# Optimization experiments

Hardware: AMD Instinct MI355X
Metric: run time of the kernel (lower is better)

The kernel has to match this reference:

```python
import jax, jax.numpy as jnp
import numpy as np

B, C, H, W = 2, 4, 32, 256   # batch, num_classes (class 0 = background), range-image H x W
N = H * W                    # candidate points per (batch, class)
RADIUS = 3.0
KM_ITERS = 1
COORD_SCALE = 60.0           # spread lidar x/y so radius-3 NMS is non-trivial


def setup_inputs() -> dict:
    key = jax.random.key(0)
    k1, k2 = jax.random.split(key)
    segmented_channels = jax.random.normal(k1, (B, C, H, W), dtype=jnp.float32)
    lidar = jax.random.normal(k2, (B, 2, H, W), dtype=jnp.float32) * COORD_SCALE
    return {"segmented_channels": segmented_channels, "lidar": lidar}


def _radius_nms(points, mask, radius):
    # Greedy radius NMS in index order: keep point i iff no earlier kept point
    # lies within `radius`. Masked-out points are never kept (keep init = mask).
    n = points.shape[0]
    idx = jnp.arange(n)
    r2 = radius * radius

    def step(keep, i):
        d2 = jnp.sum((points - points[i]) ** 2, axis=-1)       # [N]
        suppress = keep & (d2 < r2) & (idx > i) & keep[i]
        return keep & ~suppress, None

    keep, _ = jax.lax.scan(step, mask, idx)
    return keep


def _kmeans(points, mask, keep, iters):
    # Centers initialized at the NMS-kept points (same index space as points).
    # Each valid class point is assigned to nearest valid center; centers move
    # to the mean of their assigned points.
    n = points.shape[0]
    centers = points
    w = mask.astype(points.dtype)
    BIG = jnp.asarray(1e30, points.dtype)
    for _ in range(iters):
        d2 = jnp.sum((points[:, None, :] - centers[None, :, :]) ** 2, axis=-1)  # [N,N]
        d2 = jnp.where(keep[None, :], d2, BIG)
        assign = jnp.argmin(d2, axis=1)                         # [N]
        sums = jax.ops.segment_sum(points * w[:, None], assign, num_segments=n)
        cnt = jax.ops.segment_sum(w, assign, num_segments=n)
        upd = sums / jnp.maximum(cnt, 1.0)[:, None]
        centers = jnp.where((keep & (cnt > 0))[:, None], upd, centers)
    return centers * keep[:, None].astype(points.dtype)


def reference(segmented_channels, lidar):
    ind = jnp.argmax(segmented_channels, axis=1)                # [B,H,W] class id per cell
    pts = jnp.stack([lidar[:, 0], lidar[:, 1]], axis=-1).reshape(B, N, 2)
    # boolean class masks for foreground classes 1..C-1
    cls_mask = jnp.stack([ind == c for c in range(1, C)], axis=1).reshape(B, C - 1, N)
    pts_all = jnp.broadcast_to(pts[:, None], (B, C - 1, N, 2)).reshape(B * (C - 1), N, 2)
    mask_all = cls_mask.reshape(B * (C - 1), N)

    def per_bc(args):
        p, m = args
        keep = _radius_nms(p, m, RADIUS)
        centers = _kmeans(p, m, keep, KM_ITERS)
        return centers, keep

    centers, keep = jax.lax.map(per_bc, (pts_all, mask_all))
    # centers: padded [B, C-1, N, 2]; keep marks which rows are real detections
    return centers.reshape(B, C - 1, N, 2), keep.reshape(B, C - 1, N)
```

## Files before the change

kernel.cpp:

```cpp
#include <hip/hip_runtime.h>

#define NPTS 8192
#define BCLS 4
#define NP   6
#define R2   9.0f
#define RAD  3.0f
#define GRD  64
#define NCELL (GRD*GRD)
#define PCAP 2048
#define LDSK 2048

#define ST_U 0u
#define ST_A 1u
#define ST_D 2u

__global__ __launch_bounds__(1024) void k_fused(
    const float* __restrict__ seg, const float* __restrict__ lidar,
    float* __restrict__ sumx, float* __restrict__ sumy, float* __restrict__ cntw,
    float* __restrict__ out)
{
    const int p = blockIdx.x;
    const int b = p / 3, cls = p % 3 + 1;
    const int tid = threadIdx.x, lane = tid & 63, wv = tid >> 6;
    const int base = p * NPTS;

    __shared__ float2 sps[NPTS];
    __shared__ unsigned int cmb[NPTS];
    __shared__ unsigned int cellpack[NCELL];
    __shared__ unsigned short plist[2][PCAP];
    __shared__ float ksx[LDSK], ksy[LDSK], kcn[LDSK];
    __shared__ int pcnt[2];
    __shared__ unsigned long long ballots[128];
    __shared__ unsigned int base128[128];
    __shared__ unsigned int wtot[16];
    __shared__ float redbuf[4][16];
    __shared__ float sbminx, sbminy, scell;
    __shared__ int sM, sK;

    float* ok = out + (size_t)2 * NP * NPTS + base;

    for (int k = tid; k < NPTS; k += 1024) { cmb[k] = ST_U; ok[k] = 0.f; }
    {
        float2* oc = (float2*)(out + (size_t)2 * base);
        for (int k = tid; k < NPTS; k += 1024) oc[k] = make_float2(0.f, 0.f);
    }
    for (int k = tid; k < NCELL; k += 1024) cellpack[k] = 0u;
    for (int k = tid; k < LDSK; k += 1024) { ksx[k] = 0.f; ksy[k] = 0.f; kcn[k] = 0.f; }
    if (tid == 0) { pcnt[0] = 0; pcnt[1] = 0; }

    const float* segb = seg + (size_t)b * BCLS * NPTS;
    const float* lx = lidar + (size_t)b * 2 * NPTS;
    const float* ly = lx + NPTS;
    for (int c0 = 0; c0 < 8; ++c0) {
        int n = c0 * 1024 + tid;
        float bv = segb[n];
        int bc = 0;
        #pragma unroll
        for (int c2 = 1; c2 < BCLS; ++c2) {
            float v = segb[c2 * NPTS + n];
            if (v > bv) { bv = v; bc = c2; }
        }
        unsigned long long bal = __ballot(bc == cls);
        if (lane == 0) ballots[c0 * 16 + wv] = bal;
    }
    for (int n = tid; n < NPTS; n += 1024) sps[n] = make_float2(lx[n], ly[n]);
    __syncthreads();
    if (wv == 0) {
        unsigned int s = (unsigned int)__popcll(ballots[2 * lane]) +
                         (unsigned int)__popcll(ballots[2 * lane + 1]);
        for (int d = 1; d < 64; d <<= 1) s += __shfl_xor(s, d, 64);
        if (lane == 0) sM = (int)s;
    }

    const unsigned long long mw = ballots[tid >> 3];
    {
        float mnx = 3e38f, mxx = -3e38f, mny = 3e38f, mxy = -3e38f;
        #pragma unroll
        for (int q = 0; q < 8; ++q) {
            int n = tid * 8 + q;
            bool m = (mw >> (((tid & 7) << 3) + q)) & 1ull;
            float2 c = sps[n];
            if (m) {
                mnx = fminf(mnx, c.x); mxx = fmaxf(mxx, c.x);
                mny = fminf(mny, c.y); mxy = fmaxf(mxy, c.y);
            }
        }
        for (int d = 32; d; d >>= 1) {
            mnx = fminf(mnx, __shfl_xor(mnx, d, 64));
            mxx = fmaxf(mxx, __shfl_xor(mxx, d, 64));
            mny = fminf(mny, __shfl_xor(mny, d, 64));
            mxy = fmaxf(mxy, __shfl_xor(mxy, d, 64));
        }
        if (lane == 0) { redbuf[0][wv] = mnx; redbuf[1][wv] = mxx;
                         redbuf[2][wv] = mny; redbuf[3][wv] = mxy; }
    }
    __syncthreads();
    if (tid == 0) {
        float a = redbuf[0][0], b2 = redbuf[1][0], c = redbuf[2][0], d = redbuf[3][0];
        for (int q = 1; q < 16; ++q) {
            a = fminf(a, redbuf[0][q]); b2 = fmaxf(b2, redbuf[1][q]);
            c = fminf(c, redbuf[2][q]); d = fmaxf(d, redbuf[3][q]);
        }
        sbminx = a; sbminy = c;
        scell = fmaxf(2.0f * RAD, fmaxf(b2 - a, d - c) / 63.0f);
    }
    __syncthreads();
    const float bminx = sbminx, bminy = sbminy, inv = 1.0f / scell;
    const int M = sM;

    float xq[8], yq[8];
    int cellq[8];
    #pragma unroll
    for (int q = 0; q < 8; ++q) {
        int n = tid * 8 + q;
        bool m = (mw >> (((tid & 7) << 3) + q)) & 1ull;
        float2 c = sps[n];
        xq[q] = c.x; yq[q] = c.y;
        int ix = min(GRD - 1, max(0, (int)((c.x - bminx) * inv)));
        int iy = min(GRD - 1, max(0, (int)((c.y - bminy) * inv)));
        cellq[q] = m ? (iy * GRD + ix) : -1;
        if (m) atomicAdd(&cellpack[iy * GRD + ix], 1u);
    }
    __syncthreads();
    {
        unsigned int c4[4], t4 = 0;
        #pragma unroll
        for (int q = 0; q < 4; ++q) { c4[q] = cellpack[tid * 4 + q]; t4 += c4[q]; }
        unsigned int v = t4;
        for (int d = 1; d < 64; d <<= 1) {
            unsigned int u = __shfl_up(v, d, 64);
            if (lane >= d) v += u;
        }
        if (lane == 63) wtot[wv] = v;
        __syncthreads();
        if (tid == 0) {
            unsigned int acc = 0;
            for (int q = 0; q < 16; ++q) { unsigned int t = wtot[q]; wtot[q] = acc; acc += t; }
        }
        __syncthreads();
        unsigned int excl = wtot[wv] + v - t4;
        #pragma unroll
        for (int q = 0; q < 4; ++q) { cellpack[tid * 4 + q] = excl << 16; excl += c4[q]; }
    }
    __syncthreads();
    #pragma unroll
    for (int q = 0; q < 8; ++q) {
        if (cellq[q] >= 0) {
            unsigned int old = atomicAdd(&cellpack[cellq[q]], 1u);
            unsigned int pos = (old >> 16) + (old & 0xffffu);
            sps[pos] = make_float2(xq[q], yq[q]);
            cmb[pos] = ((unsigned int)(tid * 8 + q) << 2) | ST_U;
        }
    }
    __syncthreads();

    #define ROW_FLAGS(CY, CX0, CX1, NI, ME, DEAD, UNDEC)                          \
    {                                                                             \
        unsigned int wa = cellpack[(CY) * GRD + (CX0)];                           \
        unsigned int wb = cellpack[(CY) * GRD + (CX1)];                           \
        unsigned int f0 = wa >> 16, f1 = (wb >> 16) + (wb & 0xffffu);             \
        for (unsigned int f = f0; f < f1; ++f) {                                  \
            unsigned int wf = cmb[f];                                             \
            float2 q = sps[f];                                                    \
            float dx = __fsub_rn((ME).x, q.x), dy = __fsub_rn((ME).y, q.y);       \
            float d2 = __fadd_rn(__fmul_rn(dx, dx), __fmul_rn(dy, dy));           \
            bool in = (d2 < R2) & ((int)(wf >> 2) < (NI));                        \
            DEAD  |= in & ((wf & 3u) == ST_A);                                    \
            UNDEC |= in & ((wf & 3u) == ST_U);                                    \
        }                                                                         \
    }
    #define SCAN_FLAGS(NI, ME, DEAD, UNDEC)                                       \
    {                                                                             \
        int cx0 = max(0, (int)(((ME).x - RAD - bminx) * inv));                    \
        int cx1 = min(GRD - 1, (int)(((ME).x + RAD - bminx) * inv));              \
        int cy0 = max(0, (int)(((ME).y - RAD - bminy) * inv));                    \
        int cy1 = min(GRD - 1, (int)(((ME).y + RAD - bminy) * inv));              \
        DEAD = false; UNDEC = false;                                              \
        ROW_FLAGS(cy0, cx0, cx1, NI, ME, DEAD, UNDEC);                            \
        if (cy1 > cy0) ROW_FLAGS(cy1, cx0, cx1, NI, ME, DEAD, UNDEC);             \
    }

    for (int e = tid; e < M; e += 1024) {
        unsigned int w = cmb[e];
        int ni = (int)(w >> 2);
        float2 me = sps[e];
        bool dead, undec;
        SCAN_FLAGS(ni, me, dead, undec);
        if (dead) cmb[e] = (w & ~3u) | ST_D;
        else if (!undec) cmb[e] = (w & ~3u) | ST_A;
        bool pendf = !dead && undec;
        unsigned long long act = __ballot(true);
        unsigned long long bal = __ballot(pendf);
        int leader = __builtin_ctzll(act);
        int cnt = __popcll(bal);
        int wbase = 0;
        if (lane == leader && cnt) wbase = atomicAdd(&pcnt[0], cnt);
        wbase = __shfl(wbase, leader, 64);
        if (pendf) {
            int pos = wbase + __popcll(bal & ((1ull << lane) - 1ull));
            if (pos < PCAP) plist[0][pos] = (unsigned short)e;
        }
    }

    int cur = 0;
    for (int round = 0; round < NPTS; ++round) {
        __syncthreads();
        int pc = pcnt[cur];
        if (pc == 0) break;
        if (pc > PCAP) {
            for (;;) {
                bool any = false;
                __syncthreads();
                for (int e = tid; e < M; e += 1024) {
                    unsigned int w = cmb[e];
                    if ((w & 3u) != ST_U) continue;
                    int ni = (int)(w >> 2);
                    float2 me = sps[e];
                    bool dead, undec;
                    SCAN_FLAGS(ni, me, dead, undec);
                    if (dead) cmb[e] = (w & ~3u) | ST_D;
                    else if (!undec) cmb[e] = (w & ~3u) | ST_A;
                    else any = true;
                }
                if (__syncthreads_count(any) == 0) break;
            }
            break;
        }
        if (tid == 0) pcnt[cur ^ 1] = 0;
        __syncthreads();
        for (int idx = tid; idx < pc; idx += 1024) {
            int e = plist[cur][idx];
            unsigned int w = cmb[e];
            int ni = (int)(w >> 2);
            float2 me = sps[e];
            bool dead, undec;
            SCAN_FLAGS(ni, me, dead, undec);
            if (dead) cmb[e] = (w & ~3u) | ST_D;
            else if (!undec) cmb[e] = (w & ~3u) | ST_A;
            bool pendf = !dead && undec;
            unsigned long long act = __ballot(true);
            unsigned long long bal = __ballot(pendf);
            int leader = __builtin_ctzll(act);
            int cnt = __popcll(bal);
            int wbase = 0;
            if (lane == leader && cnt) wbase = atomicAdd(&pcnt[cur ^ 1], cnt);
            wbase = __shfl(wbase, leader, 64);
            if (pendf) {
                int pos = wbase + __popcll(bal & ((1ull << lane) - 1ull));
                if (pos < PCAP) plist[cur ^ 1][pos] = (unsigned short)e;
            }
        }
        cur ^= 1;
    }
    __syncthreads();

    for (int k = 0; k < 8; ++k) {
        int e = (k << 10) + tid;
        unsigned long long bal = __ballot((cmb[e] & 3u) == ST_A);
        if (lane == 0) ballots[(k << 4) + wv] = bal;
    }
    __syncthreads();
    if (wv == 0) {
        unsigned int p0 = (unsigned int)__popcll(ballots[2 * lane]);
        unsigned int p1 = (unsigned int)__popcll(ballots[2 * lane + 1]);
        unsigned int s = p0 + p1, v = s;
        for (int d = 1; d < 64; d <<= 1) {
            unsigned int u = __shfl_up(v, d, 64);
            if (lane >= d) v += u;
        }
        base128[2 * lane] = v - s;
        base128[2 * lane + 1] = v - p1;
        if (lane == 63) sK = (int)v;
    }
    __syncthreads();
    #define KRANK(E) ((int)base128[(E) >> 6] +                                    \
                      __popcll(ballots[(E) >> 6] & ((1ull << ((E) & 63)) - 1ull)))
    if (sK > LDSK) {
        for (int k = tid; k < NPTS; k += 1024) {
            sumx[base + k] = 0.f; sumy[base + k] = 0.f; cntw[base + k] = 0.f;
        }
        __syncthreads();
    }

    #define ROW_ARGMIN(CY, CX0, CX1, ME, BD, BE, BN)                              \
    {                                                                             \
        unsigned int wa = cellpack[(CY) * GRD + (CX0)];                           \
        unsigned int wb = cellpack[(CY) * GRD + (CX1)];                           \
        unsigned int f0 = wa >> 16, f1 = (wb >> 16) + (wb & 0xffffu);             \
        for (unsigned int f = f0; f < f1; ++f) {                                  \
            unsigned int wf = cmb[f];                                             \
            float2 q = sps[f];                                                    \
            float dx = __fsub_rn((ME).x, q.x), dy = __fsub_rn((ME).y, q.y);       \
            float d2 = __fadd_rn(__fmul_rn(dx, dx), __fmul_rn(dy, dy));           \
            int nf = (int)(wf >> 2);                                              \
            bool better = ((wf & 3u) == ST_A) &                                   \
                          ((d2 < BD) | ((d2 == BD) & (nf < BN)));                 \
            BD = better ? d2 : BD;                                                \
            BE = better ? (int)f : BE;                                            \
            BN = better ? nf : BN;                                                \
        }                                                                         \
    }
    for (int e = tid; e < M; e += 1024) {
        unsigned int w = cmb[e];
        float2 me = sps[e];
        int be;
        if ((w & 3u) == ST_A) {
            be = e;
        } else {
            int cx0 = max(0, (int)((me.x - RAD - bminx) * inv));
            int cx1 = min(GRD - 1, (int)((me.x + RAD - bminx) * inv));
            int cy0 = max(0, (int)((me.y - RAD - bminy) * inv));
            int cy1 = min(GRD - 1, (int)((me.y + RAD - bminy) * inv));
            float bd = 3e38f;
            be = -1;
            int bn = 1 << 30;
            ROW_ARGMIN(cy0, cx0, cx1, me, bd, be, bn);
            if (cy1 > cy0) ROW_ARGMIN(cy1, cx0, cx1, me, bd, be, bn);
            if (be < 0) continue;
        }
        int r = KRANK(be);
        if (r < LDSK) {
            atomicAdd(&ksx[r], me.x);
            atomicAdd(&ksy[r], me.y);
            atomicAdd(&kcn[r], 1.0f);
        } else {
            atomicAdd(&sumx[base + be], me.x);
            atomicAdd(&sumy[base + be], me.y);
            atomicAdd(&cntw[base + be], 1.0f);
        }
    }
    __syncthreads();

    for (int e = tid; e < M; e += 1024) {
        unsigned int w = cmb[e];
        if ((w & 3u) != ST_A) continue;
        int n = (int)(w >> 2);
        int r = KRANK(e);
        float sx, sy, c;
        if (r < LDSK) { sx = ksx[r]; sy = ksy[r]; c = kcn[r]; }
        else { sx = sumx[base + e]; sy = sumy[base + e]; c = cntw[base + e]; }
        out[2 * (base + n)]     = sx / c;
        out[2 * (base + n) + 1] = sy / c;
        ok[n] = 1.0f;
    }
}

extern "C" void kernel_launch(void* const* d_in, const int* in_sizes, int n_in,
                              void* d_out, int out_size, void* d_ws, size_t ws_size,
                              hipStream_t stream) {
    const float* seg   = (const float*)d_in[0];
    const float* lidar = (const float*)d_in[1];
    float* out = (float*)d_out;

    const size_t A = (size_t)NP * NPTS;
    float* sumx = (float*)d_ws;
    float* sumy = sumx + A;
    float* cntw = sumy + A;

    k_fused<<<NP, 1024, 0, stream>>>(seg, lidar, sumx, sumy, cntw, out);
}
```

Before: 108.0 us.

## Resolve small pending NMS sets within a single wavefront loop

When 128 or fewer points are still undecided, one wavefront now iterates their neighbor scans by itself in a loop. It repeats until every point is decided, or for up to 512 iterations. This replaces repeated block-wide rounds, each needing __syncthreads across 1024 threads, with wave-level ballots and block-scope fences. The cost is that the remaining tail runs on a single wave while the other waves sit idle. The scheme also depends on LDS writes from other lanes becoming visible within the wave under __threadfence_block.

```diff
diff --git a/kernel.cpp b/kernel.cpp
--- a/kernel.cpp
+++ b/kernel.cpp
@@ -9,6 +9,7 @@
 #define NCELL (GRD*GRD)
 #define PCAP 2048
 #define LDSK 2048
+#define WSER 128
 
 #define ST_U 0u
 #define ST_A 1u
@@ -207,6 +208,50 @@
         __syncthreads();
         int pc = pcnt[cur];
         if (pc == 0) break;
+        if (tid == 0) pcnt[cur ^ 1] = 0;
+        if (pc <= WSER) {
+            if (wv == 0) {
+                int e0 = (lane < pc) ? plist[cur][lane] : -1;
+                int e1 = (lane + 64 < pc) ? plist[cur][lane + 64] : -1;
+                int ni0 = 0, ni1 = 0;
+                float2 me0 = make_float2(0.f, 0.f), me1 = me0;
+                if (e0 >= 0) { unsigned int w = cmb[e0]; ni0 = (int)(w >> 2); me0 = sps[e0]; }
+                if (e1 >= 0) { unsigned int w = cmb[e1]; ni1 = (int)(w >> 2); me1 = sps[e1]; }
+                bool d0 = (e0 < 0), d1 = (e1 < 0);
+                int iter = 0;
+                while (__ballot((!d0) | (!d1)) != 0ull && iter < 512) {
+                    __threadfence_block();
+                    if (!d0) {
+                        bool dead, undec;
+                        SCAN_FLAGS(ni0, me0, dead, undec);
+                        if (dead)        { cmb[e0] = ((unsigned int)ni0 << 2) | ST_D; d0 = true; }
+                        else if (!undec) { cmb[e0] = ((unsigned int)ni0 << 2) | ST_A; d0 = true; }
+                    }
+                    if (!d1) {
+                        bool dead, undec;
+                        SCAN_FLAGS(ni1, me1, dead, undec);
+                        if (dead)        { cmb[e1] = ((unsigned int)ni1 << 2) | ST_D; d1 = true; }
+                        else if (!undec) { cmb[e1] = ((unsigned int)ni1 << 2) | ST_A; d1 = true; }
+                    }
+                    ++iter;
+                }
+                unsigned long long l0 = __ballot(!d0), l1 = __ballot(!d1);
+                if ((l0 | l1) != 0ull) {
+                    __threadfence_block();
+                    int cnt = __popcll(l0) + __popcll(l1);
+                    int wbase = 0;
+                    if (lane == 0) wbase = atomicAdd(&pcnt[cur ^ 1], cnt);
+                    wbase = __shfl(wbase, 0, 64);
+                    int r0 = __popcll(l0 & ((1ull << lane) - 1ull));
+                    if (!d0) plist[cur ^ 1][wbase + r0] = (unsigned short)e0;
+                    int off1 = __popcll(l0) + __popcll(l1 & ((1ull << lane) - 1ull));
+                    if (!d1) plist[cur ^ 1][wbase + off1] = (unsigned short)e1;
+                }
+            }
+            cur ^= 1;
+            continue;
+        }
+        __syncthreads();
         if (pc > PCAP) {
             for (;;) {
                 bool any = false;
@@ -226,8 +271,6 @@
             }
             break;
         }
-        if (tid == 0) pcnt[cur ^ 1] = 0;
-        __syncthreads();
         for (int idx = tid; idx < pc; idx += 1024) {
             int e = plist[cur][idx];
             unsigned int w = cmb[e];
```

New measurement: 113.3 us. +4.8%, slower.

## Iterate NMS resolution within waves and drop per-round counter reset barrier

Applied to the files above, without the earlier changes.

Pending-point counters become a per-round array, so the extra barrier that reset the next counter each round is no longer needed. Each wave also re-scans its undecided points several times within a round, stopping once no lane makes progress, so dependency chains can resolve without a block-wide barrier per step. After 62 rounds the code falls back to the full sweep loop. This adds redundant neighbour scans per wave and relies on intra-block LDS visibility through block-scope fences.

```diff
diff --git a/kernel.cpp b/kernel.cpp
--- a/kernel.cpp
+++ b/kernel.cpp
@@ -29,7 +29,7 @@
     __shared__ unsigned int cellpack[NCELL];
     __shared__ unsigned short plist[2][PCAP];
     __shared__ float ksx[LDSK], ksy[LDSK], kcn[LDSK];
-    __shared__ int pcnt[2];
+    __shared__ int pcnt2[64];
     __shared__ unsigned long long ballots[128];
     __shared__ unsigned int base128[128];
     __shared__ unsigned int wtot[16];
@@ -46,7 +46,7 @@
     }
     for (int k = tid; k < NCELL; k += 1024) cellpack[k] = 0u;
     for (int k = tid; k < LDSK; k += 1024) { ksx[k] = 0.f; ksy[k] = 0.f; kcn[k] = 0.f; }
-    if (tid == 0) { pcnt[0] = 0; pcnt[1] = 0; }
+    if (tid < 64) pcnt2[tid] = 0;
 
     const float* segb = seg + (size_t)b * BCLS * NPTS;
     const float* lx = lidar + (size_t)b * 2 * NPTS;
@@ -194,7 +194,7 @@
         int leader = __builtin_ctzll(act);
         int cnt = __popcll(bal);
         int wbase = 0;
-        if (lane == leader && cnt) wbase = atomicAdd(&pcnt[0], cnt);
+        if (lane == leader && cnt) wbase = atomicAdd(&pcnt2[0], cnt);
         wbase = __shfl(wbase, leader, 64);
         if (pendf) {
             int pos = wbase + __popcll(bal & ((1ull << lane) - 1ull));
@@ -202,12 +202,12 @@
         }
     }
 
-    int cur = 0;
-    for (int round = 0; round < NPTS; ++round) {
+    for (int round = 0; ; ++round) {
         __syncthreads();
-        int pc = pcnt[cur];
+        int pc = pcnt2[round];
         if (pc == 0) break;
-        if (pc > PCAP) {
+        int cur = round & 1;
+        if (pc > PCAP || round >= 62) {
             for (;;) {
                 bool any = false;
                 __syncthreads();
@@ -226,31 +226,36 @@
             }
             break;
         }
-        if (tid == 0) pcnt[cur ^ 1] = 0;
-        __syncthreads();
         for (int idx = tid; idx < pc; idx += 1024) {
             int e = plist[cur][idx];
             unsigned int w = cmb[e];
             int ni = (int)(w >> 2);
             float2 me = sps[e];
-            bool dead, undec;
-            SCAN_FLAGS(ni, me, dead, undec);
-            if (dead) cmb[e] = (w & ~3u) | ST_D;
-            else if (!undec) cmb[e] = (w & ~3u) | ST_A;
-            bool pendf = !dead && undec;
+            bool und = true;
+            for (int it = 0; it < 80; ++it) {
+                __threadfence_block();
+                bool progress = false;
+                if (und) {
+                    bool dead, undec;
+                    SCAN_FLAGS(ni, me, dead, undec);
+                    if (dead)        { cmb[e] = (w & ~3u) | ST_D; und = false; progress = true; }
+                    else if (!undec) { cmb[e] = (w & ~3u) | ST_A; und = false; progress = true; }
+                }
+                if (__ballot(progress) == 0ull) break;
+            }
+            bool pendf = und;
             unsigned long long act = __ballot(true);
             unsigned long long bal = __ballot(pendf);
             int leader = __builtin_ctzll(act);
             int cnt = __popcll(bal);
             int wbase = 0;
-            if (lane == leader && cnt) wbase = atomicAdd(&pcnt[cur ^ 1], cnt);
+            if (lane == leader && cnt) wbase = atomicAdd(&pcnt2[round + 1], cnt);
             wbase = __shfl(wbase, leader, 64);
             if (pendf) {
                 int pos = wbase + __popcll(bal & ((1ull << lane) - 1ull));
                 if (pos < PCAP) plist[cur ^ 1][pos] = (unsigned short)e;
             }
         }
-        cur ^= 1;
     }
     __syncthreads();
 
```

New measurement: 109.3 us. Within noise of the previous version (+1.2%).
